# Kernel tuning notes

Measured on AMD Instinct MI355X. Metric: run time of the kernel, lower is better.

## Reference

```python
import jax, jax.numpy as jnp
import numpy as np

B, T, H, IN, OUT, FUT = 256, 512, 512, 1, 1, 16


def setup_inputs() -> dict:
    key = jax.random.key(0)
    ks = jax.random.split(key, 11)
    bound = 1.0 / np.sqrt(H)  # torch LSTMCell/Linear default init
    u = lambda kk, sh: jax.random.uniform(kk, sh, jnp.float32, -bound, bound)
    fbias = lambda b: b.at[H:2 * H].set(1.0)  # forget-gate bias filled with 1.0 per __init__
    return {
        "x": jax.random.normal(ks[0], (B, T), jnp.float32),
        "Wih0": u(ks[1], (4 * H, IN)),
        "Whh0": u(ks[2], (4 * H, H)),
        "bih0": fbias(u(ks[3], (4 * H,))),
        "bhh0": fbias(u(ks[4], (4 * H,))),
        "Wih1": u(ks[5], (4 * H, H)),
        "Whh1": u(ks[6], (4 * H, H)),
        "bih1": fbias(u(ks[7], (4 * H,))),
        "bhh1": fbias(u(ks[8], (4 * H,))),
        "Wlin": u(ks[9], (OUT, H)),
        "blin": u(ks[10], (OUT,)),
        "future": FUT,
    }


def _cell(xv, h, c, Wih, Whh, bih, bhh):
    # torch.nn.LSTMCell: gates ordered (i, f, g, o)
    gates = xv @ Wih.T + h @ Whh.T + bih + bhh
    i, f, g, o = jnp.split(gates, 4, axis=-1)
    c = jax.nn.sigmoid(f) * c + jax.nn.sigmoid(i) * jnp.tanh(g)
    h = jax.nn.sigmoid(o) * jnp.tanh(c)
    return h, c


def reference(x, Wih0, Whh0, bih0, bhh0, Wih1, Whh1, bih1, bhh1, Wlin, blin, future):
    params = ((Wih0, Whh0, bih0, bhh0), (Wih1, Whh1, bih1, bhh1))
    Bsz, hid = x.shape[0], Whh0.shape[1]
    h0 = tuple(jnp.zeros((Bsz, hid), x.dtype) for _ in params)
    c0 = tuple(jnp.zeros((Bsz, hid), x.dtype) for _ in params)

    def layer_stack(inp, hs, cs):
        new_h, new_c = [], []
        for j, (Wih, Whh, bih, bhh) in enumerate(params):
            h, c = _cell(inp, hs[j], cs[j], Wih, Whh, bih, bhh)
            new_h.append(h)
            new_c.append(c)
            inp = h
        return tuple(new_h), tuple(new_c), inp

    def cond_step(carry, xt):  # xt: [B, 1]
        hs, cs = carry
        hs, cs, top = layer_stack(xt, hs, cs)
        out = top @ Wlin.T + blin  # [B, 1]
        return (hs, cs), out

    xs = jnp.swapaxes(x, 0, 1)[:, :, None]  # [T, B, 1]
    (hs, cs), outs = jax.lax.scan(cond_step, (h0, c0), xs)
    last = outs[-1]

    def fut_step(carry, _):
        hs, cs, out = carry
        hs, cs, top = layer_stack(out, hs, cs)
        out = top @ Wlin.T + blin
        return (hs, cs, out), out

    _, fut_outs = jax.lax.scan(fut_step, (hs, cs, last), None, length=future)

    all_outs = jnp.concatenate([outs, fut_outs], axis=0)  # [T+future, B, 1]
    return jnp.swapaxes(all_outs, 0, 1)[:, :, 0]  # [B, T+future]
```

## Files before the change

kernel.cpp:

```cpp
#include <hip/hip_runtime.h>
#include <hip/hip_bf16.h>
#include <math.h>

#define HID    512
#define BATCH  256
#define TLEN   512
#define FUT    16
#define NSTEP  (TLEN + FUT)
#define NGRP   16
#define WPG    16
#define BPG    16
#define UPW    32
#define NR     128

#define OFF_W0   0u
#define OFF_W1   2097152u
#define OFF_CA   6291456u
#define OFF_XF   7340032u
#define OFF_WI   7357440u
#define OFF_B0   7365632u
#define OFF_B1   7373824u
#define OFF_BAR  7382016u
#define OFF_XT   7384064u

typedef __bf16 bf16x8 __attribute__((ext_vector_type(8)));
typedef float  f32x4  __attribute__((ext_vector_type(4)));

__device__ __forceinline__ float sigf(float v)      { return 1.f / (1.f + __expf(-v)); }
__device__ __forceinline__ float tanh_fast(float v) { return 2.f / (1.f + __expf(-2.f * v)) - 1.f; }

__device__ __forceinline__ void store_short_llc(void* p, unsigned short v) {
    asm volatile("global_store_short %0, %1, off sc0 sc1"
                 :: "v"(p), "v"((unsigned)v) : "memory");
}

__device__ __forceinline__ void gl2lds16_llc(const void* g, void* l) {
    __builtin_amdgcn_global_load_lds(
        (const __attribute__((address_space(1))) void*)g,
        (__attribute__((address_space(3))) void*)l, 16, 0, 17);
}

__device__ __forceinline__ void flag_barrier(unsigned* flags, int m, unsigned phase) {
    __builtin_amdgcn_s_waitcnt(0);
    __syncthreads();
    if (threadIdx.x == 0)
        __hip_atomic_store(&flags[m], phase, __ATOMIC_RELAXED, __HIP_MEMORY_SCOPE_AGENT);
    if (threadIdx.x < 64) {
        const int lane = threadIdx.x;
        const bool active = (lane < WPG) && (lane != m);
        for (;;) {
            unsigned f = phase;
            if (active)
                f = __hip_atomic_load(&flags[lane], __ATOMIC_RELAXED, __HIP_MEMORY_SCOPE_AGENT);
            if (__ballot(f >= phase) == ~0ull) break;
            __builtin_amdgcn_s_sleep(1);
        }
    }
    __syncthreads();
}

__global__ void lstm_init(char* __restrict__ ws, float* __restrict__ out,
                          const float* __restrict__ blin)
{
    float bl = blin[0];
    int tid = blockIdx.x * blockDim.x + threadIdx.x;
    int stride = gridDim.x * blockDim.x;
    uint4* ca = (uint4*)(ws + OFF_CA);
    for (int i = tid; i < 65536; i += stride) ca[i] = make_uint4(0u, 0u, 0u, 0u);
    float* xf = (float*)(ws + OFF_XF);
    for (int i = tid; i < (FUT + 1) * BATCH; i += stride) xf[i] = bl;
    unsigned* bar = (unsigned*)(ws + OFF_BAR);
    for (int i = tid; i < NGRP * 32; i += stride) bar[i] = 0u;
    for (int i = tid; i < BATCH * NSTEP; i += stride) out[i] = bl;
}

__global__ void lstm_pack(char* __restrict__ ws,
    const float* __restrict__ x,
    const float* __restrict__ Wih0, const float* __restrict__ Whh0,
    const float* __restrict__ bih0, const float* __restrict__ bhh0,
    const float* __restrict__ Wih1, const float* __restrict__ Whh1,
    const float* __restrict__ bih1, const float* __restrict__ bhh1)
{
    int tid = blockIdx.x * blockDim.x + threadIdx.x;
    int stride = gridDim.x * blockDim.x;

    __hip_bfloat16* W0p = (__hip_bfloat16*)(ws + OFF_W0);
    for (int i = tid; i < 16 * 128 * 512; i += stride) {
        int k = i & 511, r = (i >> 9) & 127, m = i >> 16;
        int row = (r >> 5) * HID + m * UPW + (r & 31);
        W0p[i] = __float2bfloat16(Whh0[(size_t)row * HID + k]);
    }
    __hip_bfloat16* W1p = (__hip_bfloat16*)(ws + OFF_W1);
    for (int i = tid; i < 16 * 128 * 1024; i += stride) {
        int k = i & 1023, r = (i >> 10) & 127, m = i >> 17;
        int row = (r >> 5) * HID + m * UPW + (r & 31);
        float v = (k < 512) ? Wih1[(size_t)row * HID + k] : Whh1[(size_t)row * HID + (k - 512)];
        W1p[i] = __float2bfloat16(v);
    }
    float* wi = (float*)(ws + OFF_WI);
    float* b0 = (float*)(ws + OFF_B0);
    float* b1 = (float*)(ws + OFF_B1);
    for (int i = tid; i < 16 * 128; i += stride) {
        int r = i & 127, m = i >> 7;
        int row = (r >> 5) * HID + m * UPW + (r & 31);
        wi[i] = Wih0[row];
        b0[i] = bih0[row] + bhh0[row];
        b1[i] = bih1[row] + bhh1[row];
    }
    float* xT = (float*)(ws + OFF_XT);
    for (int i = tid; i < TLEN * BATCH; i += stride) {
        int t = i >> 8, b = i & 255;
        xT[i] = x[(size_t)b * TLEN + t];
    }
}

__global__ __launch_bounds__(512, 2) void lstm_persist(
    const float* __restrict__ wlin,
    float* __restrict__ out, char* __restrict__ ws)
{
    const int tid  = threadIdx.x;
    const int lane = tid & 63;
    const int wave = tid >> 6;
    const int g    = blockIdx.x & 15;
    const int m    = blockIdx.x >> 4;
    const int bbase = g * BPG;

    __shared__ __attribute__((aligned(16))) __hip_bfloat16 As[16 * 1024];
    __shared__ float g0S[16][136];
    __shared__ float g1S[16][136];
    char* AsB = (char*)As;

    {
        int* az = (int*)As;
        for (int i = tid; i < (16 * 1024 * 2) / 4; i += 512) az[i] = 0;
    }

    const float* wis = (const float*)(ws + OFF_WI) + m * NR;
    const float* b0s = (const float*)(ws + OFF_B0) + m * NR;
    const float* b1s = (const float*)(ws + OFF_B1) + m * NR;
    char* CAg = ws + OFF_CA + (size_t)g * 65536;
    float* xfeed = (float*)(ws + OFF_XF);
    const float* xT = (const float*)(ws + OFF_XT);
    unsigned* flags = (unsigned*)(ws + OFF_BAR) + g * 32;

    const int fl = lane & 15;
    const int fq = lane >> 4;
    const int w  = wave;
    const int us  = tid & 31;
    const int b0r = tid >> 5;

    const float wl0 = wlin[m * UPW + us];
    float wiR[4], b0R[4], b1R[4];
#pragma unroll
    for (int q = 0; q < 4; ++q) {
        wiR[q] = wis[q * 32 + us];
        b0R[q] = b0s[q * 32 + us];
        b1R[q] = b1s[q * 32 + us];
    }
    float c00 = 0.f, c10 = 0.f;

    const int cgr  = 4 * m + (us >> 3);
    const int pub0 = b0r * 1024 + (((cgr + b0r) & 63) << 4) + (us & 7) * 2;

    const bf16x8* W0row = (const bf16x8*)(ws + OFF_W0 + (size_t)m * NR * 512 * 2)
                          + (size_t)(w * 16 + fl) * 64;
    const bf16x8* W1row = (const bf16x8*)(ws + OFF_W1 + (size_t)m * NR * 1024 * 2)
                          + (size_t)(w * 16 + fl) * 128;
    bf16x8 w0f[16], w1f[32];
#pragma unroll
    for (int ks = 0; ks < 16; ++ks) w0f[ks] = W0row[ks * 4 + fq];
#pragma unroll
    for (int ks = 0; ks < 32; ++ks) w1f[ks] = W1row[ks * 4 + fq];

    __syncthreads();

    const bf16x8* Asv = (const bf16x8*)As;

    unsigned phase = 0;
    for (int t = 0; t < NSTEP; ++t) {
        const int p = t & 1;
        char* CAp = CAg + p * 32768;
        char* CAq = CAg + (1 - p) * 32768;

        float xv0;
        if (t < TLEN) {
            xv0 = xT[t * BATCH + bbase + b0r];
        } else {
            xv0 = xfeed[(t - TLEN) * BATCH + bbase + b0r];
        }

        f32x4 acc0 = {0.f, 0.f, 0.f, 0.f};
#pragma unroll
        for (int ks = 0; ks < 16; ++ks) {
            int c = ks * 4 + fq;
            bf16x8 a0 = Asv[fl * 128 + ((c + fl) & 63)];
            acc0 = __builtin_amdgcn_mfma_f32_16x16x32_bf16(a0, w0f[ks], acc0, 0, 0, 0);
        }
#pragma unroll
        for (int i = 0; i < 4; ++i)
            g0S[fq * 4 + i][w * 16 + fl] = acc0[i];
        __syncthreads();

        {
            float gi = g0S[b0r][us]      + b0R[0] + xv0 * wiR[0];
            float gf = g0S[b0r][32 + us] + b0R[1] + xv0 * wiR[1];
            float gg = g0S[b0r][64 + us] + b0R[2] + xv0 * wiR[2];
            float go = g0S[b0r][96 + us] + b0R[3] + xv0 * wiR[3];
            c00 = sigf(gf) * c00 + sigf(gi) * tanh_fast(gg);
            __hip_bfloat16 h = __float2bfloat16(sigf(go) * tanh_fast(c00));
            store_short_llc(CAp + pub0, *(unsigned short*)&h);
        }

        ++phase;
        flag_barrier(flags, m, phase);

        {
#pragma unroll
            for (int ci = 0; ci < 2; ++ci) {
                int b = wave * 2 + ci;
                gl2lds16_llc(CAp + b * 1024 + lane * 16,
                             AsB + b * 2048 + lane * 16);
                gl2lds16_llc(CAq + 16384 + b * 1024 + lane * 16,
                             AsB + b * 2048 + 1024 + lane * 16);
            }
            __builtin_amdgcn_s_waitcnt(0);
            __syncthreads();
        }

        acc0 = (f32x4){0.f, 0.f, 0.f, 0.f};
#pragma unroll
        for (int ks = 0; ks < 16; ++ks) {
            int c = ks * 4 + fq;
            bf16x8 a0 = Asv[fl * 128 + ((c + fl) & 63)];
            acc0 = __builtin_amdgcn_mfma_f32_16x16x32_bf16(a0, w1f[ks], acc0, 0, 0, 0);
        }
#pragma unroll
        for (int ks = 16; ks < 32; ++ks) {
            int c = (ks - 16) * 4 + fq;
            bf16x8 a0 = Asv[fl * 128 + 64 + ((c + fl) & 63)];
            acc0 = __builtin_amdgcn_mfma_f32_16x16x32_bf16(a0, w1f[ks], acc0, 0, 0, 0);
        }
#pragma unroll
        for (int i = 0; i < 4; ++i)
            g1S[fq * 4 + i][w * 16 + fl] = acc0[i];
        __syncthreads();

        {
            float gi = g1S[b0r][us]      + b1R[0];
            float gf = g1S[b0r][32 + us] + b1R[1];
            float gg = g1S[b0r][64 + us] + b1R[2];
            float go = g1S[b0r][96 + us] + b1R[3];
            c10 = sigf(gf) * c10 + sigf(gi) * tanh_fast(gg);
            float h = sigf(go) * tanh_fast(c10);
            __hip_bfloat16 hb = __float2bfloat16(h);
            store_short_llc(CAp + 16384 + pub0, *(unsigned short*)&hb);
            float po = wl0 * h;
#pragma unroll
            for (int off = 1; off < 32; off <<= 1) po += __shfl_xor(po, off, 64);
            if (us == 0) {
                atomicAdd(&out[(size_t)(bbase + b0r) * NSTEP + t], po);
                if (t >= TLEN - 1)
                    atomicAdd(&xfeed[(t - (TLEN - 1)) * BATCH + bbase + b0r], po);
            }
        }

        if (t >= TLEN - 1) {
            ++phase;
            flag_barrier(flags, m, phase);
        }
    }
}

extern "C" void kernel_launch(void* const* d_in, const int* in_sizes, int n_in,
                              void* d_out, int out_size, void* d_ws, size_t ws_size,
                              hipStream_t stream)
{
    const float* x    = (const float*)d_in[0];
    const float* Wih0 = (const float*)d_in[1];
    const float* Whh0 = (const float*)d_in[2];
    const float* bih0 = (const float*)d_in[3];
    const float* bhh0 = (const float*)d_in[4];
    const float* Wih1 = (const float*)d_in[5];
    const float* Whh1 = (const float*)d_in[6];
    const float* bih1 = (const float*)d_in[7];
    const float* bhh1 = (const float*)d_in[8];
    const float* Wlin = (const float*)d_in[9];
    const float* blin = (const float*)d_in[10];
    float* out = (float*)d_out;
    char* ws = (char*)d_ws;

    hipLaunchKernelGGL(lstm_init, dim3(256), dim3(256), 0, stream, ws, out, blin);
    hipLaunchKernelGGL(lstm_pack, dim3(512), dim3(256), 0, stream,
                       ws, x, Wih0, Whh0, bih0, bhh0, Wih1, Whh1, bih1, bhh1);
    hipLaunchKernelGGL(lstm_persist, dim3(256), dim3(512), 0, stream, Wlin, out, ws);
}
```

Measured before the change: 2.360 ms.

## Split K across wave halves and give each wave two row tiles with partial-sum reduction

Each wave now computes two 16-row output tiles over half of the K dimension instead of one tile over the full K, so every A fragment loaded from LDS feeds two MFMAs. The two K-halves write partial sums into a shared buffer that is summed during the gate activations. This halves the LDS A-fragment reads per MFMA and gives two independent accumulator chains per wave. In exchange it adds an extra LDS buffer and extra adds in the activation step, plus a __syncthreads at the end of each non-future step to guard reuse of that buffer. Launch bounds are switched to explicit amdgpu attributes pinning two waves per EU.

```diff
diff --git a/kernel.cpp b/kernel.cpp
--- a/kernel.cpp
+++ b/kernel.cpp
@@ -114,7 +114,9 @@
     }
 }
 
-__global__ __launch_bounds__(512, 2) void lstm_persist(
+__global__ __attribute__((amdgpu_flat_work_group_size(512, 512),
+                          amdgpu_waves_per_eu(2, 2)))
+void lstm_persist(
     const float* __restrict__ wlin,
     float* __restrict__ out, char* __restrict__ ws)
 {
@@ -126,8 +128,7 @@
     const int bbase = g * BPG;
 
     __shared__ __attribute__((aligned(16))) __hip_bfloat16 As[16 * 1024];
-    __shared__ float g0S[16][136];
-    __shared__ float g1S[16][136];
+    __shared__ float gp[2][16][140];
     char* AsB = (char*)As;
 
     {
@@ -145,7 +146,8 @@
 
     const int fl = lane & 15;
     const int fq = lane >> 4;
-    const int w  = wave;
+    const int kh = wave >> 2;
+    const int wq = wave & 3;
     const int us  = tid & 31;
     const int b0r = tid >> 5;
 
@@ -162,15 +164,19 @@
     const int cgr  = 4 * m + (us >> 3);
     const int pub0 = b0r * 1024 + (((cgr + b0r) & 63) << 4) + (us & 7) * 2;
 
-    const bf16x8* W0row = (const bf16x8*)(ws + OFF_W0 + (size_t)m * NR * 512 * 2)
-                          + (size_t)(w * 16 + fl) * 64;
-    const bf16x8* W1row = (const bf16x8*)(ws + OFF_W1 + (size_t)m * NR * 1024 * 2)
-                          + (size_t)(w * 16 + fl) * 128;
-    bf16x8 w0f[16], w1f[32];
-#pragma unroll
-    for (int ks = 0; ks < 16; ++ks) w0f[ks] = W0row[ks * 4 + fq];
-#pragma unroll
-    for (int ks = 0; ks < 32; ++ks) w1f[ks] = W1row[ks * 4 + fq];
+    const bf16x8* W0base = (const bf16x8*)(ws + OFF_W0 + (size_t)m * NR * 512 * 2);
+    const bf16x8* W1base = (const bf16x8*)(ws + OFF_W1 + (size_t)m * NR * 1024 * 2);
+    bf16x8 w0f[2][8], w1f[2][16];
+#pragma unroll
+    for (int rt = 0; rt < 2; ++rt) {
+        const int row = (wq * 2 + rt) * 16 + fl;
+#pragma unroll
+        for (int j = 0; j < 8; ++j)
+            w0f[rt][j] = W0base[(size_t)row * 64 + (kh * 8 + j) * 4 + fq];
+#pragma unroll
+        for (int j = 0; j < 16; ++j)
+            w1f[rt][j] = W1base[(size_t)row * 128 + (kh * 16 + j) * 4 + fq];
+    }
 
     __syncthreads();
 
@@ -190,22 +196,26 @@
         }
 
         f32x4 acc0 = {0.f, 0.f, 0.f, 0.f};
-#pragma unroll
-        for (int ks = 0; ks < 16; ++ks) {
-            int c = ks * 4 + fq;
+        f32x4 acc1 = {0.f, 0.f, 0.f, 0.f};
+#pragma unroll
+        for (int j = 0; j < 8; ++j) {
+            const int c = kh * 32 + j * 4 + fq;
             bf16x8 a0 = Asv[fl * 128 + ((c + fl) & 63)];
-            acc0 = __builtin_amdgcn_mfma_f32_16x16x32_bf16(a0, w0f[ks], acc0, 0, 0, 0);
-        }
-#pragma unroll
-        for (int i = 0; i < 4; ++i)
-            g0S[fq * 4 + i][w * 16 + fl] = acc0[i];
+            acc0 = __builtin_amdgcn_mfma_f32_16x16x32_bf16(a0, w0f[0][j], acc0, 0, 0, 0);
+            acc1 = __builtin_amdgcn_mfma_f32_16x16x32_bf16(a0, w0f[1][j], acc1, 0, 0, 0);
+        }
+#pragma unroll
+        for (int i = 0; i < 4; ++i) {
+            gp[kh][fq * 4 + i][(wq * 2 + 0) * 16 + fl] = acc0[i];
+            gp[kh][fq * 4 + i][(wq * 2 + 1) * 16 + fl] = acc1[i];
+        }
         __syncthreads();
 
         {
-            float gi = g0S[b0r][us]      + b0R[0] + xv0 * wiR[0];
-            float gf = g0S[b0r][32 + us] + b0R[1] + xv0 * wiR[1];
-            float gg = g0S[b0r][64 + us] + b0R[2] + xv0 * wiR[2];
-            float go = g0S[b0r][96 + us] + b0R[3] + xv0 * wiR[3];
+            float gi = gp[0][b0r][us]      + gp[1][b0r][us]      + b0R[0] + xv0 * wiR[0];
+            float gf = gp[0][b0r][32 + us] + gp[1][b0r][32 + us] + b0R[1] + xv0 * wiR[1];
+            float gg = gp[0][b0r][64 + us] + gp[1][b0r][64 + us] + b0R[2] + xv0 * wiR[2];
+            float go = gp[0][b0r][96 + us] + gp[1][b0r][96 + us] + b0R[3] + xv0 * wiR[3];
             c00 = sigf(gf) * c00 + sigf(gi) * tanh_fast(gg);
             __hip_bfloat16 h = __float2bfloat16(sigf(go) * tanh_fast(c00));
             store_short_llc(CAp + pub0, *(unsigned short*)&h);
@@ -228,28 +238,26 @@
         }
 
         acc0 = (f32x4){0.f, 0.f, 0.f, 0.f};
-#pragma unroll
-        for (int ks = 0; ks < 16; ++ks) {
-            int c = ks * 4 + fq;
-            bf16x8 a0 = Asv[fl * 128 + ((c + fl) & 63)];
-            acc0 = __builtin_amdgcn_mfma_f32_16x16x32_bf16(a0, w1f[ks], acc0, 0, 0, 0);
-        }
-#pragma unroll
-        for (int ks = 16; ks < 32; ++ks) {
-            int c = (ks - 16) * 4 + fq;
-            bf16x8 a0 = Asv[fl * 128 + 64 + ((c + fl) & 63)];
-            acc0 = __builtin_amdgcn_mfma_f32_16x16x32_bf16(a0, w1f[ks], acc0, 0, 0, 0);
-        }
-#pragma unroll
-        for (int i = 0; i < 4; ++i)
-            g1S[fq * 4 + i][w * 16 + fl] = acc0[i];
+        acc1 = (f32x4){0.f, 0.f, 0.f, 0.f};
+#pragma unroll
+        for (int j = 0; j < 16; ++j) {
+            const int c = j * 4 + fq;
+            bf16x8 a0 = Asv[fl * 128 + kh * 64 + ((c + fl) & 63)];
+            acc0 = __builtin_amdgcn_mfma_f32_16x16x32_bf16(a0, w1f[0][j], acc0, 0, 0, 0);
+            acc1 = __builtin_amdgcn_mfma_f32_16x16x32_bf16(a0, w1f[1][j], acc1, 0, 0, 0);
+        }
+#pragma unroll
+        for (int i = 0; i < 4; ++i) {
+            gp[kh][fq * 4 + i][(wq * 2 + 0) * 16 + fl] = acc0[i];
+            gp[kh][fq * 4 + i][(wq * 2 + 1) * 16 + fl] = acc1[i];
+        }
         __syncthreads();
 
         {
-            float gi = g1S[b0r][us]      + b1R[0];
-            float gf = g1S[b0r][32 + us] + b1R[1];
-            float gg = g1S[b0r][64 + us] + b1R[2];
-            float go = g1S[b0r][96 + us] + b1R[3];
+            float gi = gp[0][b0r][us]      + gp[1][b0r][us]      + b1R[0];
+            float gf = gp[0][b0r][32 + us] + gp[1][b0r][32 + us] + b1R[1];
+            float gg = gp[0][b0r][64 + us] + gp[1][b0r][64 + us] + b1R[2];
+            float go = gp[0][b0r][96 + us] + gp[1][b0r][96 + us] + b1R[3];
             c10 = sigf(gf) * c10 + sigf(gi) * tanh_fast(gg);
             float h = sigf(go) * tanh_fast(c10);
             __hip_bfloat16 hb = __float2bfloat16(h);
@@ -267,6 +275,8 @@
         if (t >= TLEN - 1) {
             ++phase;
             flag_barrier(flags, m, phase);
+        } else {
+            __syncthreads();
         }
     }
 }
```

Result: faster. 2.201 ms (-6.7%).
